# Kernel tuning notes

Measured on AMD Instinct MI355X. Metric: run time of the kernel, lower is better.

The kernel has to match this reference:

```python
import jax, jax.numpy as jnp
import numpy as np


def setup_inputs() -> dict:
    key = jax.random.key(0)
    k1, k2, k3, k4 = jax.random.split(key, 4)
    B, n_latent, n_donors, n_out = 16384, 128, 500, 128
    u = jax.random.normal(k1, (B, n_latent), dtype=jnp.float32)
    donor_id = jax.random.randint(k2, (B,), 0, n_donors, dtype=jnp.int64)
    amat_sample = jax.random.normal(k3, (n_donors, n_latent, n_out), dtype=jnp.float32)
    offsets = jax.random.normal(k4, (n_donors, n_out), dtype=jnp.float32)
    return {"u": u, "donor_id": donor_id, "amat_sample": amat_sample, "offsets": offsets}


def reference(u, donor_id, amat_sample, offsets):
    # Gather per-sample weight slice [B, n_latent, n_out] and offsets [B, n_out]
    As = amat_sample[donor_id]
    u_det = jax.lax.stop_gradient(u)  # original uses u.detach() for delta path
    # per-sample mat-vec: (As * u[..., None]).sum(-2)
    z2 = jnp.einsum('blo,bl->bo', As, u_det)
    delta = z2 + offsets[donor_id]
    return u + delta
```

## Files before the change

kernel.cpp:

```cpp
#include <hip/hip_runtime.h>
#include <hip/hip_bf16.h>

#define N_LATENT 128
#define N_OUT    128
#define SLCAP    128
#define CAPU     64
#define MAXI     8

typedef __bf16 bf16x4 __attribute__((ext_vector_type(4)));
typedef __bf16 bf16x8 __attribute__((ext_vector_type(8)));
typedef float  f32x4  __attribute__((ext_vector_type(4)));

__global__ __launch_bounds__(512, 4) void ldz_kernel(
    const float* __restrict__ u,
    const int*   __restrict__ donor_id,
    const float* __restrict__ amat,
    const float* __restrict__ offsets,
    float*       __restrict__ out,
    int B)
{
    const int d    = blockIdx.x;
    const int t    = threadIdx.x;
    const int wave = t >> 6;
    const int lane = t & 63;
    const int q    = lane >> 4;
    const int c16  = lane & 15;
    const int o    = wave * 16 + c16;
    const int c    = t & 31;

    __shared__ int scount;
    __shared__ int slist[SLCAP];
    __shared__ __align__(16) char usb[CAPU * 256];

    if (t == 0) scount = 0;

    const int4* did4 = (const int4*)donor_id;
    const int nq = B >> 2;
    int4 idv[MAXI];
    #pragma unroll
    for (int p = 0; p < MAXI; ++p) {
        const int i = t + p * 512;
        if (i < nq) idv[p] = did4[i];
    }

    float bv[4][8];
    const float* abase = amat + (size_t)d * (N_LATENT * N_OUT) + o;
    #pragma unroll
    for (int ks = 0; ks < 4; ++ks)
        #pragma unroll
        for (int i = 0; i < 8; ++i)
            bv[ks][i] = __builtin_nontemporal_load(
                abase + (size_t)(ks * 32 + q * 8 + i) * N_OUT);

    const float off = offsets[(size_t)d * N_OUT + o];

    __syncthreads();

    #pragma unroll
    for (int p = 0; p < MAXI; ++p) {
        const int i = t + p * 512;
        if (i < nq) {
            int4 v = idv[p];
            int b = 4 * i;
            if (v.x == d) { int pp = atomicAdd(&scount, 1); if (pp < SLCAP) slist[pp] = b; }
            if (v.y == d) { int pp = atomicAdd(&scount, 1); if (pp < SLCAP) slist[pp] = b + 1; }
            if (v.z == d) { int pp = atomicAdd(&scount, 1); if (pp < SLCAP) slist[pp] = b + 2; }
            if (v.w == d) { int pp = atomicAdd(&scount, 1); if (pp < SLCAP) slist[pp] = b + 3; }
        }
    }
    __syncthreads();
    const int n  = min(scount, SLCAP);
    const int nl = min(n, CAPU);

    float4 ur[4];
    #pragma unroll
    for (int p = 0; p < 4; ++p) {
        const int r = (t >> 5) + p * 16;
        ur[p] = (r < nl) ? *(const float4*)(u + (size_t)slist[r] * N_LATENT + c * 4)
                         : make_float4(0.f, 0.f, 0.f, 0.f);
    }

    bf16x8 bfr[4];
    #pragma unroll
    for (int ks = 0; ks < 4; ++ks) {
        bf16x8 f;
        #pragma unroll
        for (int i = 0; i < 8; ++i) f[i] = (__bf16)bv[ks][i];
        bfr[ks] = f;
    }

    #pragma unroll
    for (int p = 0; p < 4; ++p) {
        const int r = (t >> 5) + p * 16;
        if (r < nl) {
            bf16x4 w = { (__bf16)ur[p].x, (__bf16)ur[p].y, (__bf16)ur[p].z, (__bf16)ur[p].w };
            *(bf16x4*)(usb + r * 256 + ((c * 8) ^ ((r & 15) << 4))) = w;
        }
    }
    __syncthreads();

    for (int m0 = 0; m0 < nl; m0 += 16) {
        const int m = m0 + c16;
        f32x4 acc = {0.f, 0.f, 0.f, 0.f};
        #pragma unroll
        for (int ks = 0; ks < 4; ++ks) {
            bf16x8 af = *(const bf16x8*)(usb + m * 256 +
                                         ((ks * 64 + q * 16) ^ (c16 << 4)));
            acc = __builtin_amdgcn_mfma_f32_16x16x32_bf16(af, bfr[ks], acc, 0, 0, 0);
        }
        #pragma unroll
        for (int r = 0; r < 4; ++r) {
            const int s = m0 + q * 4 + r;
            if (s < nl) {
                float uv = (float)*(const __bf16*)(usb + s * 256 +
                                                   ((o * 2) ^ ((s & 15) << 4)));
                __builtin_nontemporal_store(uv + off + acc[r],
                                            out + (size_t)slist[s] * N_OUT + o);
            }
        }
    }

    for (int s2 = CAPU + wave; s2 < n; s2 += 8) {
        const int b = slist[s2];
        #pragma unroll
        for (int half = 0; half < 2; ++half) {
            const int o2 = half * 64 + lane;
            float acc = 0.f;
            for (int l = 0; l < N_LATENT; ++l)
                acc = fmaf(u[(size_t)b * N_LATENT + l],
                           amat[(size_t)d * N_LATENT * N_OUT + (size_t)l * N_OUT + o2],
                           acc);
            out[(size_t)b * N_OUT + o2] =
                u[(size_t)b * N_LATENT + o2] + offsets[(size_t)d * N_OUT + o2] + acc;
        }
    }
}

extern "C" void kernel_launch(void* const* d_in, const int* in_sizes, int n_in,
                              void* d_out, int out_size, void* d_ws, size_t ws_size,
                              hipStream_t stream) {
    const float* u        = (const float*)d_in[0];
    const int*   donor_id = (const int*)d_in[1];
    const float* amat     = (const float*)d_in[2];
    const float* offsets  = (const float*)d_in[3];
    float*       out      = (float*)d_out;

    const int B        = in_sizes[1];
    const int n_donors = in_sizes[3] / N_OUT;

    hipLaunchKernelGGL(ldz_kernel, dim3(n_donors), dim3(512), 0, stream,
                       u, donor_id, amat, offsets, out, B);
}
```

Before: 15.21 us.

## Bin samples by donor in a separate kernel before per-donor matvec

Each per-donor block used to scan the whole donor_id array and collect matching samples through shared-memory atomics. A separate binning kernel now does one global-atomic pass that builds per-donor index lists in the workspace, and the matvec kernel just reads its list and count. This removes the redundant full scan each block did, at the cost of a memset, two extra launches and global atomic contention. The result ordering within bins becomes nondeterministic, which does not affect the output.

Result: slower. 25.22 us (+65.8%).

```diff
diff --git a/kernel.cpp b/kernel.cpp
--- a/kernel.cpp
+++ b/kernel.cpp
@@ -3,21 +3,31 @@
 
 #define N_LATENT 128
 #define N_OUT    128
-#define SLCAP    128
+#define BIN_CAP  128
 #define CAPU     64
-#define MAXI     8
 
 typedef __bf16 bf16x4 __attribute__((ext_vector_type(4)));
 typedef __bf16 bf16x8 __attribute__((ext_vector_type(8)));
 typedef float  f32x4  __attribute__((ext_vector_type(4)));
 
-__global__ __launch_bounds__(512, 4) void ldz_kernel(
+__global__ void bin_kernel(const int* __restrict__ donor_id,
+                           int* __restrict__ cnt, int* __restrict__ bins, int B)
+{
+    int b = blockIdx.x * 256 + threadIdx.x;
+    if (b < B) {
+        int d = donor_id[b];
+        int pos = atomicAdd(&cnt[d], 1);
+        if (pos < BIN_CAP) bins[d * BIN_CAP + pos] = b;
+    }
+}
+
+__global__ __launch_bounds__(512, 4) void matvec_kernel(
     const float* __restrict__ u,
-    const int*   __restrict__ donor_id,
     const float* __restrict__ amat,
     const float* __restrict__ offsets,
-    float*       __restrict__ out,
-    int B)
+    const int*   __restrict__ cnt,
+    const int*   __restrict__ bins,
+    float*       __restrict__ out)
 {
     const int d    = blockIdx.x;
     const int t    = threadIdx.x;
@@ -28,20 +38,11 @@
     const int o    = wave * 16 + c16;
     const int c    = t & 31;
 
-    __shared__ int scount;
-    __shared__ int slist[SLCAP];
+    __shared__ int slist[BIN_CAP];
     __shared__ __align__(16) char usb[CAPU * 256];
 
-    if (t == 0) scount = 0;
-
-    const int4* did4 = (const int4*)donor_id;
-    const int nq = B >> 2;
-    int4 idv[MAXI];
-    #pragma unroll
-    for (int p = 0; p < MAXI; ++p) {
-        const int i = t + p * 512;
-        if (i < nq) idv[p] = did4[i];
-    }
+    const int myidx = (t < BIN_CAP) ? bins[d * BIN_CAP + t] : 0;
+    const int cntv  = cnt[d];
 
     float bv[4][8];
     const float* abase = amat + (size_t)d * (N_LATENT * N_OUT) + o;
@@ -54,22 +55,9 @@
 
     const float off = offsets[(size_t)d * N_OUT + o];
 
+    if (t < BIN_CAP) slist[t] = myidx;
     __syncthreads();
-
-    #pragma unroll
-    for (int p = 0; p < MAXI; ++p) {
-        const int i = t + p * 512;
-        if (i < nq) {
-            int4 v = idv[p];
-            int b = 4 * i;
-            if (v.x == d) { int pp = atomicAdd(&scount, 1); if (pp < SLCAP) slist[pp] = b; }
-            if (v.y == d) { int pp = atomicAdd(&scount, 1); if (pp < SLCAP) slist[pp] = b + 1; }
-            if (v.z == d) { int pp = atomicAdd(&scount, 1); if (pp < SLCAP) slist[pp] = b + 2; }
-            if (v.w == d) { int pp = atomicAdd(&scount, 1); if (pp < SLCAP) slist[pp] = b + 3; }
-        }
-    }
-    __syncthreads();
-    const int n  = min(scount, SLCAP);
+    const int n  = min(cntv, BIN_CAP);
     const int nl = min(n, CAPU);
 
     float4 ur[4];
@@ -148,6 +136,12 @@
     const int B        = in_sizes[1];
     const int n_donors = in_sizes[3] / N_OUT;
 
-    hipLaunchKernelGGL(ldz_kernel, dim3(n_donors), dim3(512), 0, stream,
-                       u, donor_id, amat, offsets, out, B);
+    int* cnt  = (int*)d_ws;
+    int* bins = (int*)((char*)d_ws + 4096);
+
+    hipMemsetAsync(cnt, 0, (size_t)n_donors * sizeof(int), stream);
+    hipLaunchKernelGGL(bin_kernel, dim3((B + 255) / 256), dim3(256), 0, stream,
+                       donor_id, cnt, bins, B);
+    hipLaunchKernelGGL(matvec_kernel, dim3(n_donors), dim3(512), 0, stream,
+                       u, amat, offsets, cnt, bins, out);
 }
```
